# Performance work log

Hardware: AMD Instinct MI355X
Metric: run time of the kernel (lower is better)

## Reference

```python
import jax, jax.numpy as jnp
from jax import lax
import numpy as np

B, T, D, H = 64, 291, 300, 10
K = D // H  # 30
SLOPE = 0.01  # nn.LeakyReLU default
EPS = 1e-5


def _leaky(x):
    return jnp.where(x >= 0, x, SLOPE * x)


def _ln2d(x, g, b):
    # torch LayerNorm over the LAST TWO dims (normalized_shape=[t, d])
    mu = jnp.mean(x, axis=(-2, -1), keepdims=True)
    var = jnp.mean((x - mu) ** 2, axis=(-2, -1), keepdims=True)
    return (x - mu) / jnp.sqrt(var + EPS) * g + b


def _mha(x, Wq, Wk, Wv, Wm):
    # manual multi-head self-attention; q,k each scaled by h**-0.25
    b, t, d = x.shape
    s = H ** 0.25
    q = (x @ Wq.T).reshape(b, t, H, K) / s
    k = (x @ Wk.T).reshape(b, t, H, K) / s
    v = (x @ Wv.T).reshape(b, t, H, K)
    att = jax.nn.softmax(jnp.einsum('bihk,bjhk->bhij', q, k), axis=-1)
    o = jnp.einsum('bhij,bjhk->bihk', att, v).reshape(b, t, d)
    return o @ Wm.T


def _conv_head(R, W, b):
    # Conv2d(2,25,(kh,300)) valid -> [B,25,L,1]; leaky; global maxpool over L
    y = lax.conv_general_dilated(R, W, (1, 1), 'VALID',
                                 dimension_numbers=('NCHW', 'OIHW', 'NCHW'))
    y = _leaky(y + b[None, :, None, None])
    return jnp.max(y, axis=(2, 3))  # [B,25]


def setup_inputs() -> dict:
    key = jax.random.key(0)
    ks = jax.random.split(key, 32)
    it = iter(range(32))
    def n(shape, scale=0.05):
        return (jax.random.normal(ks[next(it)], shape, dtype=jnp.float32) * scale)
    inp = {
        'x1': jax.random.normal(ks[next(it)], (B, T, D), dtype=jnp.float32),
        'x2': jax.random.normal(ks[next(it)], (B, 1000), dtype=jnp.float32),
        'W_img': n((300, 1000)), 'b_img': jnp.zeros((300,), jnp.float32),
        'g1': jnp.ones((T, D), jnp.float32), 'be1': jnp.zeros((T, D), jnp.float32),
        'g2': jnp.ones((1, D), jnp.float32), 'be2': jnp.zeros((1, D), jnp.float32),
        'Wq_tp': n((D, D)), 'Wk_tp': n((D, D)), 'Wv_tp': n((D, D)),
        'Wq_pt': n((D, D)), 'Wk_pt': n((D, D)), 'Wv_pt': n((D, D)),
        'Wq1': n((D, D)), 'Wk1': n((D, D)), 'Wv1': n((D, D)), 'Wm1': n((D, D)),
        'Wq2': n((D, D)), 'Wk2': n((D, D)), 'Wv2': n((D, D)), 'Wm2': n((D, D)),
        'Wq3': n((D, D)), 'Wk3': n((D, D)), 'Wv3': n((D, D)), 'Wm3': n((D, D)),
        'Wc1': n((25, 2, 1, D)), 'Wc2': n((25, 2, 2, D)),
        'Wc3': n((25, 2, 3, D)), 'Wc4': n((25, 2, 4, D)),
        'bc1': jnp.zeros((25,), jnp.float32), 'bc2': jnp.zeros((25,), jnp.float32),
        'bc3': jnp.zeros((25,), jnp.float32), 'bc4': jnp.zeros((25,), jnp.float32),
        'Wlin': n((300, 100)), 'blin': jnp.zeros((300,), jnp.float32),
        'Wlast': n((2, 600)), 'blast': jnp.zeros((2,), jnp.float32),
    }
    return inp


def reference(x1, x2, W_img, b_img, g1, be1, g2, be2,
              Wq_tp, Wk_tp, Wv_tp, Wq_pt, Wk_pt, Wv_pt,
              Wq1, Wk1, Wv1, Wm1, Wq2, Wk2, Wv2, Wm2, Wq3, Wk3, Wv3, Wm3,
              Wc1, Wc2, Wc3, Wc4, bc1, bc2, bc3, bc4,
              Wlin, blin, Wlast, blast):
    # image branch: x2 is the frozen VGG19 1000-d encoding
    img = _leaky(x2 @ W_img.T + b_img)[:, None, :]      # [B,1,300]
    lnP = _ln2d(img, g2, be2)                           # [B,1,300]
    lnT = _ln2d(x1, g1, be1)                            # [B,291,300]

    # cross-attn T->P (query from image, kv from text), unscaled
    q = lnP @ Wq_tp.T; k = lnT @ Wk_tp.T; v = lnT @ Wv_tp.T
    a = jax.nn.softmax(jnp.einsum('bqd,btd->bqt', q, k), axis=-1)
    R_T_P = jnp.einsum('bqt,btd->bqd', a, v) + lnP      # [B,1,300]

    # cross-attn P->T (query from text, kv from image; softmax over size-1 dim)
    q = lnT @ Wq_pt.T; k = lnP @ Wk_pt.T; v = lnP @ Wv_pt.T
    a = jax.nn.softmax(jnp.einsum('btd,bqd->btq', q, k), axis=-1)
    R_P_T = jnp.einsum('btq,bqd->btd', a, v) + lnT      # [B,291,300]

    # 3 stacked multi-head self-attn blocks on the text stream
    a1 = _mha(lnT, Wq1, Wk1, Wv1, Wm1)
    a2 = _mha(a1, Wq2, Wk2, Wv2, Wm2)
    a3 = _mha(a2, Wq3, Wk3, Wv3, Wm3)

    R = jnp.stack((R_P_T, a3), axis=1)                  # [B,2,291,300]
    r1 = _conv_head(R, Wc1, bc1)
    r2 = _conv_head(R, Wc2, bc2)
    r3 = _conv_head(R, Wc3, bc3)
    r4 = _conv_head(R, Wc4, bc4)
    total = jnp.concatenate([r1, r2, r3, r4], axis=1)   # [B,100]
    total = _leaky(total @ Wlin.T + blin)               # [B,300]

    Y = jnp.concatenate([R_T_P[:, 0, :], total], axis=1) @ Wlast.T + blast
    return Y                                            # [B,2]
```

## Files before the change

kernel.cpp:

```cpp
#include <hip/hip_runtime.h>
#include <hip/hip_bf16.h>
#include <math.h>

#define Bn 64
#define Tn 291
#define Dn 300
#define Hn 10
#define Mn (Bn*Tn)
#define Mp 18688
#define Kp 320

typedef __bf16 bf16x8 __attribute__((ext_vector_type(8)));
typedef float f32x4 __attribute__((ext_vector_type(4)));

static __device__ __forceinline__ float leaky(float x){ return x >= 0.f ? x : 0.01f*x; }

template<int NT>
static __device__ __forceinline__ float blockSum(float v, float* red){
  __syncthreads();
  int lane = threadIdx.x & 63, wid = threadIdx.x >> 6;
  #pragma unroll
  for (int o = 32; o > 0; o >>= 1) v += __shfl_down(v, o, 64);
  if (lane == 0) red[wid] = v;
  __syncthreads();
  if (threadIdx.x == 0) {
    float s = red[0];
    #pragma unroll
    for (int w = 1; w < NT/64; ++w) s += red[w];
    red[0] = s;
  }
  __syncthreads();
  return red[0];
}

template<int NT>
static __device__ __forceinline__ float blockMax(float v, float* red){
  __syncthreads();
  int lane = threadIdx.x & 63, wid = threadIdx.x >> 6;
  #pragma unroll
  for (int o = 32; o > 0; o >>= 1) v = fmaxf(v, __shfl_down(v, o, 64));
  if (lane == 0) red[wid] = v;
  __syncthreads();
  if (threadIdx.x == 0) {
    float s = red[0];
    #pragma unroll
    for (int w = 1; w < NT/64; ++w) s = fmaxf(s, red[w]);
    red[0] = s;
  }
  __syncthreads();
  return red[0];
}

__global__ __launch_bounds__(256)
void k_img_lnp(const float* __restrict__ x2, const float* __restrict__ Wimg,
               const float* __restrict__ bimg, const float* __restrict__ g2,
               const float* __restrict__ be2, float* __restrict__ lnP)
{
  int b = blockIdx.x, tid = threadIdx.x;
  __shared__ float sx[1000];
  __shared__ float sy[300];
  __shared__ float red[4];
  for (int i = tid; i < 1000; i += 256) sx[i] = x2[b*1000 + i];
  __syncthreads();
  for (int j = tid; j < 300; j += 256) {
    const float* w = Wimg + j*1000;
    float a = 0.f;
    for (int i = 0; i < 1000; ++i) a += sx[i]*w[i];
    sy[j] = leaky(a + bimg[j]);
  }
  __syncthreads();
  float s = 0.f, ss = 0.f;
  for (int j = tid; j < 300; j += 256) { float v = sy[j]; s += v; ss += v*v; }
  float tot  = blockSum<256>(s, red);
  float tot2 = blockSum<256>(ss, red);
  float mu   = tot * (1.f/300.f);
  float var  = tot2 * (1.f/300.f) - mu*mu;
  float rstd = rsqrtf(var + 1e-5f);
  for (int j = tid; j < 300; j += 256)
    lnP[b*300 + j] = (sy[j]-mu)*rstd*g2[j] + be2[j];
}

__global__ __launch_bounds__(1024)
void k_lnT(const float* __restrict__ x1, const float* __restrict__ g1,
           const float* __restrict__ be1, float* __restrict__ outf,
           __hip_bfloat16* __restrict__ outb)
{
  int b = blockIdx.x, tid = threadIdx.x;
  __shared__ float red[16];
  const float4* xb = (const float4*)(x1 + (size_t)b*87300);
  const float4* g4 = (const float4*)g1;
  const float4* b4 = (const float4*)be1;
  float4* o4 = (float4*)(outf + (size_t)b*87300);
  float s = 0.f, ss = 0.f;
  for (int i = tid; i < 21825; i += 1024) {
    float4 v = xb[i];
    s  += v.x+v.y+v.z+v.w;
    ss += v.x*v.x+v.y*v.y+v.z*v.z+v.w*v.w;
  }
  float tot  = blockSum<1024>(s, red);
  float tot2 = blockSum<1024>(ss, red);
  float mu   = tot / 87300.f;
  float var  = tot2 / 87300.f - mu*mu;
  float rstd = rsqrtf(var + 1e-5f);
  for (int i = tid; i < 21825; i += 1024) {
    float4 v = xb[i], g = g4[i], be = b4[i], o;
    o.x = (v.x-mu)*rstd*g.x + be.x;
    o.y = (v.y-mu)*rstd*g.y + be.y;
    o.z = (v.z-mu)*rstd*g.z + be.z;
    o.w = (v.w-mu)*rstd*g.w + be.w;
    o4[i] = o;
  }
  const float* xs = x1 + (size_t)b*87300;
  for (int e = tid; e < Tn*Dn; e += 1024) {
    int t = e/300;
    float x = xs[e];
    outb[(size_t)(b*Tn+t)*Kp + (e - t*300)] = __float2bfloat16((x-mu)*rstd*g1[e] + be1[e]);
  }
  for (int e = tid; e < Tn*20; e += 1024) {
    int t = e/20, d = 300 + e%20;
    outb[(size_t)(b*Tn+t)*Kp + d] = __float2bfloat16(0.f);
  }
}

__global__ __launch_bounds__(320)
void k_tp(const float* __restrict__ lnP, const float* __restrict__ lnT,
          const float* __restrict__ Wq, const float* __restrict__ Wk,
          const float* __restrict__ Wv, const float* __restrict__ Wvpt,
          float* __restrict__ RTP, float* __restrict__ vpt)
{
  int b = blockIdx.x, tid = threadIdx.x;
  __shared__ float sP[300], sQ[300], sM[300], sA[291], sW[300], red[5];
  if (tid < 300) sP[tid] = lnP[b*300 + tid];
  __syncthreads();
  if (tid < 300) {
    const float* w = Wq + tid*300;
    float a = 0.f;
    for (int i = 0; i < 300; ++i) a += sP[i]*w[i];
    sQ[tid] = a;
  }
  __syncthreads();
  if (tid < 300) {
    float a = 0.f;
    for (int j = 0; j < 300; ++j) a += sQ[j]*Wk[j*300 + tid];
    sM[tid] = a;
  }
  __syncthreads();
  float sc = -1e30f;
  if (tid < 291) {
    const float* r = lnT + ((size_t)b*Tn + tid)*300;
    float a = 0.f;
    for (int i = 0; i < 300; ++i) a += r[i]*sM[i];
    sc = a;
  }
  float mx  = blockMax<320>(sc, red);
  float e   = (tid < 291) ? __expf(sc - mx) : 0.f;
  float den = blockSum<320>(e, red);
  if (tid < 291) sA[tid] = e;
  __syncthreads();
  if (tid < 300) {
    float a = 0.f;
    for (int t = 0; t < 291; ++t) a += sA[t]*lnT[((size_t)b*Tn + t)*300 + tid];
    sW[tid] = a / den;
  }
  __syncthreads();
  if (tid < 300) {
    const float* w = Wv + tid*300;
    float a = 0.f;
    for (int i = 0; i < 300; ++i) a += sW[i]*w[i];
    RTP[b*300 + tid] = a + sP[tid];
    const float* w2 = Wvpt + tid*300;
    float a2 = 0.f;
    for (int i = 0; i < 300; ++i) a2 += sP[i]*w2[i];
    vpt[b*300 + tid] = a2;
  }
}

__global__ __launch_bounds__(256)
void k_rptb(const float* __restrict__ lnT, const float* __restrict__ vpt,
            __hip_bfloat16* __restrict__ out)
{
  int idx = blockIdx.x*256 + threadIdx.x;
  if (idx >= Mn*Kp) return;
  int m = idx / Kp, d = idx - m*Kp;
  int b = m / Tn;
  float v = (d < 300) ? lnT[(size_t)m*300 + d] + vpt[b*300 + d] : 0.f;
  out[idx] = __float2bfloat16(v);
}

struct Wptrs { const float* p[12]; };

__global__ __launch_bounds__(256)
void k_wqkv(Wptrs wp, __hip_bfloat16* __restrict__ out)
{
  int idx = blockIdx.x*256 + threadIdx.x;
  if (idx >= 3*1024*Kp) return;
  int l = idx / (1024*Kp);
  int rem = idx - l*(1024*Kp);
  int rowp = rem / Kp, c = rem - rowp*Kp;
  int hh = rowp >> 5, j = rowp & 31;
  float v = 0.f;
  if (j < 30 && c < 300 && hh < 30) {
    int g = hh/10;
    v = wp.p[l*3 + g][((hh - g*10)*30 + j)*300 + c];
  }
  out[idx] = __float2bfloat16(v);
}

__global__ __launch_bounds__(256)
void k_wcvt(Wptrs wp, __hip_bfloat16* __restrict__ out, int nmat)
{
  int idx = blockIdx.x*256 + threadIdx.x;
  if (idx >= nmat*Kp*Kp) return;
  int mat = idx / (Kp*Kp);
  int rem = idx - mat*(Kp*Kp);
  int r = rem / Kp, c = rem - r*Kp;
  float v = (r < 300 && c < 300) ? wp.p[mat][r*300 + c] : 0.f;
  out[idx] = __float2bfloat16(v);
}

__global__ __launch_bounds__(256)
void k_wpackb(const float* __restrict__ Wc1, const float* __restrict__ Wc2,
              const float* __restrict__ Wc3, const float* __restrict__ Wc4,
              __hip_bfloat16* __restrict__ out)
{
  int idx = blockIdx.x*256 + threadIdx.x;
  if (idx >= 2*256*Kp) return;
  int c  = idx % Kp;
  int rc = idx / Kp;
  int ch = rc / 256;
  int r  = rc % 256;
  float v = 0.f;
  if (r < 250 && c < 300) {
    const float* W; int kh, ro;
    if      (r < 25)  { W = Wc1; kh = 1; ro = r;      }
    else if (r < 75)  { W = Wc2; kh = 2; ro = r - 25; }
    else if (r < 150) { W = Wc3; kh = 3; ro = r - 75; }
    else              { W = Wc4; kh = 4; ro = r - 150;}
    int o = ro/kh, dh = ro%kh;
    v = W[((o*2 + ch)*kh + dh)*300 + c];
  }
  out[idx] = __float2bfloat16(v);
}

template<bool PANEL>
__global__ __launch_bounds__(256)
void k_gemm3(const ushort* __restrict__ A0, const ushort* __restrict__ A1,
             const ushort* __restrict__ W0, const ushort* __restrict__ W1,
             ushort* __restrict__ C0, ushort* __restrict__ C1,
             int nn, int cpitch)
{
  const ushort* A = blockIdx.z ? A1 : A0;
  const ushort* W = blockIdx.z ? W1 : W0;
  ushort*       C = blockIdx.z ? C1 : C0;
  int total = gridDim.x;
  int bid = blockIdx.x;
  int q = total >> 3, r = total & 7;
  int xcd = bid & 7, idx = bid >> 3;
  int wgid = (xcd < r ? xcd*(q+1) : r*(q+1) + (xcd-r)*q) + idx;
  int m0 = (wgid / nn) * 128, n0 = (wgid % nn) * 64;

  __shared__ alignas(16) ushort As[2][128*64];
  __shared__ alignas(16) ushort Bs[2][64*64];
  int tid = threadIdx.x;
  int lane = tid & 63, w = tid >> 6, wr = w >> 1, wc = w & 1;
  int lm = lane & 15, lk = lane >> 4;
  f32x4 acc[4][2] = {};
  uint4 ra[4], rw[2];

  auto loadregs = [&](int kt){
    #pragma unroll
    for (int u = 0; u < 4; ++u) {
      int s = tid + u*256; int row = s >> 3, kg = s & 7;
      ra[u] = *(const uint4*)(A + (size_t)(m0+row)*Kp + kt*64 + kg*8);
    }
    #pragma unroll
    for (int u = 0; u < 2; ++u) {
      int s = tid + u*256; int row = s >> 3, kg = s & 7;
      rw[u] = *(const uint4*)(W + (size_t)(n0+row)*Kp + kt*64 + kg*8);
    }
  };
  auto writeLDS = [&](int buf){
    #pragma unroll
    for (int u = 0; u < 4; ++u) {
      int s = tid + u*256; int row = s >> 3, kg = s & 7;
      *(uint4*)&As[buf][row*64 + ((kg ^ (row&7)) << 3)] = ra[u];
    }
    #pragma unroll
    for (int u = 0; u < 2; ++u) {
      int s = tid + u*256; int row = s >> 3, kg = s & 7;
      *(uint4*)&Bs[buf][row*64 + ((kg ^ (row&7)) << 3)] = rw[u];
    }
  };
  auto compute = [&](int buf){
    #pragma unroll
    for (int s = 0; s < 2; ++s) {
      bf16x8 af[4], bfr[2];
      int kg = s*4 + lk;
      #pragma unroll
      for (int mf = 0; mf < 4; ++mf) {
        int rr = wr*64 + mf*16 + lm;
        af[mf] = *(const bf16x8*)&As[buf][rr*64 + ((kg ^ (rr&7)) << 3)];
      }
      #pragma unroll
      for (int nf = 0; nf < 2; ++nf) {
        int rr = wc*32 + nf*16 + lm;
        bfr[nf] = *(const bf16x8*)&Bs[buf][rr*64 + ((kg ^ (rr&7)) << 3)];
      }
      #pragma unroll
      for (int mf = 0; mf < 4; ++mf)
        #pragma unroll
        for (int nf = 0; nf < 2; ++nf)
          acc[mf][nf] = __builtin_amdgcn_mfma_f32_16x16x32_bf16(af[mf], bfr[nf], acc[mf][nf], 0, 0, 0);
    }
  };

  loadregs(0); writeLDS(0);
  __syncthreads();
  #pragma unroll 1
  for (int kt = 0; kt < 5; ++kt) {
    if (kt < 4) loadregs(kt+1);
    compute(kt & 1);
    if (kt < 4) {
      __syncthreads();
      writeLDS((kt+1) & 1);
      __syncthreads();
    }
  }
  __syncthreads();
  ushort* T = &As[0][0];
  #pragma unroll
  for (int mf = 0; mf < 4; ++mf)
    #pragma unroll
    for (int nf = 0; nf < 2; ++nf)
      #pragma unroll
      for (int i = 0; i < 4; ++i) {
        int rr = wr*64 + mf*16 + lk*4 + i;
        int cc = wc*32 + nf*16 + lm;
        __hip_bfloat16 t = __float2bfloat16(acc[mf][nf][i]);
        T[rr*72 + cc] = *(ushort*)&t;
      }
  __syncthreads();
  #pragma unroll
  for (int u = 0; u < 4; ++u) {
    int s = tid + u*256; int row = s >> 3, g = s & 7;
    uint4 v = *(const uint4*)&T[row*72 + g*8];
    if (PANEL)
      *(uint4*)(C + ((size_t)(n0 >> 6)*Mp + m0 + row)*64 + g*8) = v;
    else
      *(uint4*)(C + (size_t)(m0+row)*cpitch + n0 + g*8) = v;
  }
}

__global__ __launch_bounds__(256)
void k_attn6(const ushort* __restrict__ Xp, ushort* __restrict__ O)
{
  int b = blockIdx.x, h = blockIdx.y, tid = threadIdx.x;
  __shared__ alignas(16) ushort Ks[320*40];
  __shared__ alignas(16) ushort Vt[32*328];
  __shared__ alignas(16) ushort Ps[64*168];
  const size_t rb = (size_t)b*Tn;
  const int Pq = h >> 1, off = (h & 1)*32;
  const int hq = h*30;
  for (int i = tid; i < 320*16; i += 256) {
    int r = i >> 4, c2 = i & 15;
    uint v = (r < Tn) ? *(const uint*)(Xp + ((size_t)(5+Pq)*Mp + rb + r)*64 + off + 2*c2) : 0u;
    *(uint*)&Ks[r*40 + 2*c2] = v;
  }
  for (int i = tid; i < 320*16; i += 256) {
    int j = i >> 4, c2 = i & 15;
    uint v = (j < Tn) ? *(const uint*)(Xp + ((size_t)(10+Pq)*Mp + rb + j)*64 + off + 2*c2) : 0u;
    Vt[(2*c2)*328 + j]   = (ushort)(v & 0xffffu);
    Vt[(2*c2+1)*328 + j] = (ushort)(v >> 16);
  }
  __syncthreads();
  int lane = tid & 63, w = tid >> 6;
  int lm = lane & 15, lk = lane >> 4;
  int qloc = w*16 + lm;
  const float scale = 0.31622776601683794f;
  #pragma unroll 1
  for (int qt = 0; qt < 5; ++qt) {
    int qrow = qt*64 + w*16 + lm;
    union { uint u[4]; bf16x8 v; } qq;
    {
      const uint* qp = (const uint*)(Xp + ((size_t)Pq*Mp + rb + qrow)*64 + off + lk*8);
      qq.u[0]=qp[0]; qq.u[1]=qp[1]; qq.u[2]=qp[2]; qq.u[3]=qp[3];
    }
    bf16x8 qf = qq.v;
    float rsum = 0.f;
    f32x4 oacc[2] = {};
    #pragma unroll 1
    for (int jh = 0; jh < 2; ++jh) {
      #pragma unroll
      for (int jtl = 0; jtl < 10; ++jtl) {
        int jt = jh*10 + jtl;
        bf16x8 kf = *(const bf16x8*)&Ks[(jt*16+lm)*40 + lk*8];
        f32x4 s = {};
        s = __builtin_amdgcn_mfma_f32_16x16x32_bf16(kf, qf, s, 0, 0, 0);
        union { ushort u[4]; uint2 v2; } pk;
        #pragma unroll
        for (int i2 = 0; i2 < 4; ++i2) {
          int j = jt*16 + lk*4 + i2;
          float p = (j < Tn) ? __expf(s[i2]*scale) : 0.f;
          rsum += p;
          __hip_bfloat16 t = __float2bfloat16(p);
          pk.u[i2] = *(ushort*)&t;
        }
        *(uint2*)&Ps[qloc*168 + jtl*16 + lk*4] = pk.v2;
      }
      #pragma unroll
      for (int ktl = 0; ktl < 5; ++ktl) {
        bf16x8 pf = *(const bf16x8*)&Ps[qloc*168 + ktl*32 + lk*8];
        int jb = jh*160 + ktl*32 + lk*8;
        #pragma unroll
        for (int nf = 0; nf < 2; ++nf) {
          bf16x8 vf = *(const bf16x8*)&Vt[(nf*16+lm)*328 + jb];
          oacc[nf] = __builtin_amdgcn_mfma_f32_16x16x32_bf16(pf, vf, oacc[nf], 0, 0, 0);
        }
      }
    }
    rsum += __shfl_xor(rsum, 16, 64);
    rsum += __shfl_xor(rsum, 32, 64);
    float inv[4];
    #pragma unroll
    for (int i2 = 0; i2 < 4; ++i2) inv[i2] = 1.f / __shfl(rsum, lk*4 + i2, 64);
    #pragma unroll
    for (int nf = 0; nf < 2; ++nf) {
      int d = nf*16 + lm;
      if (d < 30) {
        #pragma unroll
        for (int i2 = 0; i2 < 4; ++i2) {
          int qrw = qt*64 + w*16 + lk*4 + i2;
          if (qrw < Tn) {
            __hip_bfloat16 t = __float2bfloat16(oacc[nf][i2]*inv[i2]);
            O[(rb + qrw)*Kp + hq + d] = *(ushort*)&t;
          }
        }
      }
    }
  }
}

__global__ __launch_bounds__(256)
void k_convred2(const ushort* __restrict__ G0, const ushort* __restrict__ G1,
                const float* __restrict__ bc1, const float* __restrict__ bc2,
                const float* __restrict__ bc3, const float* __restrict__ bc4,
                float* __restrict__ out100)
{
  int b = blockIdx.x, head = blockIdx.y;
  int kh  = head + 1;
  int off = (head == 0) ? 0 : (head == 1) ? 25 : (head == 2) ? 75 : 150;
  const float* bc = (head == 0) ? bc1 : (head == 1) ? bc2 : (head == 2) ? bc3 : bc4;
  int ncol = 25*kh;
  int ncp  = ncol | 1;
  int L = Tn - kh + 1;
  __shared__ float S[67*101];
  int tid = threadIdx.x, lane = tid & 63;
  float mx[7];
  #pragma unroll
  for (int u = 0; u < 7; ++u) mx[u] = -1e30f;
  for (int l0 = 0; l0 < L; l0 += 64) {
    int nrows = min(64 + kh - 1, Tn - l0);
    __syncthreads();
    for (int i = tid; i < nrows*ncol; i += 256) {
      int r = i / ncol, c = i % ncol;
      size_t g = (size_t)(b*Tn + l0 + r)*256 + off + c;
      __hip_bfloat16 a = *(const __hip_bfloat16*)&G0[g];
      __hip_bfloat16 d = *(const __hip_bfloat16*)&G1[g];
      S[r*ncp + c] = __bfloat162float(a) + __bfloat162float(d);
    }
    __syncthreads();
    int lmax = min(64, L - l0);
    #pragma unroll
    for (int u = 0; u < 7; ++u) {
      int o = (tid >> 6) + u*4;
      int dl = lane;
      if (o < 25 && dl < lmax) {
        float s = bc[o];
        for (int dh = 0; dh < kh; ++dh)
          s += S[(dl+dh)*ncp + o*kh + dh];
        mx[u] = fmaxf(mx[u], leaky(s));
      }
    }
  }
  #pragma unroll
  for (int u = 0; u < 7; ++u) {
    float v = mx[u];
    #pragma unroll
    for (int ofs = 32; ofs > 0; ofs >>= 1) v = fmaxf(v, __shfl_down(v, ofs, 64));
    int o = (tid >> 6) + u*4;
    if (lane == 0 && o < 25)
      out100[b*100 + head*25 + o] = v;
  }
}

__global__ __launch_bounds__(320)
void k_final(const float* __restrict__ RTP, const float* __restrict__ out100,
             const float* __restrict__ Wlin, const float* __restrict__ blin,
             const float* __restrict__ Wlast, const float* __restrict__ blast,
             float* __restrict__ Y)
{
  int b = blockIdx.x, tid = threadIdx.x;
  __shared__ float cat[600];
  __shared__ float s100[100];
  __shared__ float red[5];
  if (tid < 100) s100[tid] = out100[b*100 + tid];
  if (tid < 300) cat[tid] = RTP[b*300 + tid];
  __syncthreads();
  if (tid < 300) {
    const float* w = Wlin + tid*100;
    float a = blin[tid];
    for (int j = 0; j < 100; ++j) a += s100[j]*w[j];
    cat[300 + tid] = leaky(a);
  }
  __syncthreads();
  for (int c = 0; c < 2; ++c) {
    float a = 0.f;
    for (int i = tid; i < 600; i += 320) a += cat[i]*Wlast[c*600 + i];
    a = blockSum<320>(a, red);
    if (tid == 0) Y[b*2 + c] = a + blast[c];
  }
}

extern "C" void kernel_launch(void* const* d_in, const int* in_sizes, int n_in,
                              void* d_out, int out_size, void* d_ws, size_t ws_size,
                              hipStream_t stream)
{
  (void)in_sizes; (void)n_in; (void)out_size; (void)ws_size;
  const float* x1    = (const float*)d_in[0];
  const float* x2    = (const float*)d_in[1];
  const float* Wimg  = (const float*)d_in[2];
  const float* bimg  = (const float*)d_in[3];
  const float* g1    = (const float*)d_in[4];
  const float* be1   = (const float*)d_in[5];
  const float* g2    = (const float*)d_in[6];
  const float* be2   = (const float*)d_in[7];
  const float* Wq_tp = (const float*)d_in[8];
  const float* Wk_tp = (const float*)d_in[9];
  const float* Wv_tp = (const float*)d_in[10];
  const float* Wv_pt = (const float*)d_in[13];
  const float* Wc1 = (const float*)d_in[26];
  const float* Wc2 = (const float*)d_in[27];
  const float* Wc3 = (const float*)d_in[28];
  const float* Wc4 = (const float*)d_in[29];
  const float* bc1 = (const float*)d_in[30];
  const float* bc2 = (const float*)d_in[31];
  const float* bc3 = (const float*)d_in[32];
  const float* bc4 = (const float*)d_in[33];
  const float* Wlin  = (const float*)d_in[34];
  const float* blin  = (const float*)d_in[35];
  const float* Wlast = (const float*)d_in[36];
  const float* blast = (const float*)d_in[37];

  char* base = (char*)d_ws;
  float* lnP    = (float*)(base + 0);
  float* RTP    = (float*)(base + 76800);
  float* vpt    = (float*)(base + 153600);
  float* out100 = (float*)(base + 230400);
  float*  lnTf  = (float*)(base + 262144);
  ushort* X1024 = (ushort*)(base + 262144);
  ushort* G0    = (ushort*)(base + 262144);
  ushort* G1    = (ushort*)(base + 262144 + 9568256);
  ushort* P0    = (ushort*)(base + 38535168);
  ushort* P1    = (ushort*)(base + 50495488);
  ushort* P2    = (ushort*)(base + 62455808);
  ushort* Wpad  = (ushort*)(base + 74416128);
  ushort* Wm    = (ushort*)(base + 76382208);
  ushort* Wpb   = (ushort*)(base + 76996608);
  const int WS = Kp*Kp;

  k_img_lnp<<<Bn, 256, 0, stream>>>(x2, Wimg, bimg, g2, be2, lnP);
  k_lnT<<<Bn, 1024, 0, stream>>>(x1, g1, be1, lnTf, (__hip_bfloat16*)P0);
  k_tp<<<Bn, 320, 0, stream>>>(lnP, lnTf, Wq_tp, Wk_tp, Wv_tp, Wv_pt, RTP, vpt);
  k_rptb<<<(Mn*Kp + 255)/256, 256, 0, stream>>>(lnTf, vpt, (__hip_bfloat16*)P1);

  Wptrs wq;
  wq.p[0]=(const float*)d_in[14]; wq.p[1]=(const float*)d_in[15]; wq.p[2]=(const float*)d_in[16];
  wq.p[3]=(const float*)d_in[18]; wq.p[4]=(const float*)d_in[19]; wq.p[5]=(const float*)d_in[20];
  wq.p[6]=(const float*)d_in[22]; wq.p[7]=(const float*)d_in[23]; wq.p[8]=(const float*)d_in[24];
  k_wqkv<<<(3*1024*Kp + 255)/256, 256, 0, stream>>>(wq, (__hip_bfloat16*)Wpad);
  Wptrs wm;
  wm.p[0]=(const float*)d_in[17]; wm.p[1]=(const float*)d_in[21]; wm.p[2]=(const float*)d_in[25];
  k_wcvt<<<(3*WS + 255)/256, 256, 0, stream>>>(wm, (__hip_bfloat16*)Wm, 3);
  k_wpackb<<<(2*256*Kp + 255)/256, 256, 0, stream>>>(Wc1, Wc2, Wc3, Wc4, (__hip_bfloat16*)Wpb);

  dim3 gqkv(146*16, 1, 1), gproj(146*5, 1, 1), gconv(146*4, 1, 2), gat(Bn, Hn);
  for (int l = 0; l < 3; ++l) {
    const ushort* Wq3 = Wpad + (size_t)l*1024*Kp;
    const ushort* Wm3 = Wm + (size_t)l*WS;
    k_gemm3<true ><<<gqkv, 256, 0, stream>>>(P0, P0, Wq3, Wq3, X1024, X1024, 16, 0);
    k_attn6<<<gat, 256, 0, stream>>>(X1024, P2);
    k_gemm3<false><<<gproj, 256, 0, stream>>>(P2, P2, Wm3, Wm3, P0, P0, 5, 320);
  }
  k_gemm3<false><<<gconv, 256, 0, stream>>>(P1, P0, Wpb, Wpb + 256*Kp, G0, G1, 4, 256);
  k_convred2<<<dim3(Bn,4), 256, 0, stream>>>(G0, G1, bc1, bc2, bc3, bc4, out100);
  k_final<<<Bn, 320, 0, stream>>>(RTP, out100, Wlin, blin, Wlast, blast, (float*)d_out);
}
```

Baseline: 853.0 us.

## Switch activations to 64-column panel layout and rewrite GEMM with resident A tile

All bf16 activation buffers now use a panel-major layout (64-column panels of Mp rows) via a pidx helper, so every producer and consumer is updated. The GEMM is rewritten so each block loads a full 64x320 A tile into LDS once, and each wave loops over 64-wide N panels. B fragments stream directly from global memory into registers with one-step prefetch, and output goes through a small per-wave LDS staging buffer. The aim is to reuse A across all N panels and drop the double-buffered K loop and its barriers. In exchange, B is read from global memory without LDS sharing across waves, and the grid shrinks to a fixed 292x2, which may cut occupancy and parallelism.

```diff
diff --git a/kernel.cpp b/kernel.cpp
--- a/kernel.cpp
+++ b/kernel.cpp
@@ -14,6 +14,10 @@
 typedef float f32x4 __attribute__((ext_vector_type(4)));
 
 static __device__ __forceinline__ float leaky(float x){ return x >= 0.f ? x : 0.01f*x; }
+
+static __device__ __forceinline__ size_t pidx(int m, int c){
+  return ((size_t)(c >> 6)*Mp + m)*64 + (c & 63);
+}
 
 template<int NT>
 static __device__ __forceinline__ float blockSum(float v, float* red){
@@ -112,13 +116,13 @@
   }
   const float* xs = x1 + (size_t)b*87300;
   for (int e = tid; e < Tn*Dn; e += 1024) {
-    int t = e/300;
+    int t = e/300, d = e - t*300;
     float x = xs[e];
-    outb[(size_t)(b*Tn+t)*Kp + (e - t*300)] = __float2bfloat16((x-mu)*rstd*g1[e] + be1[e]);
+    outb[pidx(b*Tn + t, d)] = __float2bfloat16((x-mu)*rstd*g1[e] + be1[e]);
   }
   for (int e = tid; e < Tn*20; e += 1024) {
     int t = e/20, d = 300 + e%20;
-    outb[(size_t)(b*Tn+t)*Kp + d] = __float2bfloat16(0.f);
+    outb[pidx(b*Tn + t, d)] = __float2bfloat16(0.f);
   }
 }
 
@@ -184,7 +188,7 @@
   int m = idx / Kp, d = idx - m*Kp;
   int b = m / Tn;
   float v = (d < 300) ? lnT[(size_t)m*300 + d] + vpt[b*300 + d] : 0.f;
-  out[idx] = __float2bfloat16(v);
+  out[pidx(m, d)] = __float2bfloat16(v);
 }
 
 struct Wptrs { const float* p[12]; };
@@ -242,112 +246,79 @@
   out[idx] = __float2bfloat16(v);
 }
 
-template<bool PANEL>
-__global__ __launch_bounds__(256)
-void k_gemm3(const ushort* __restrict__ A0, const ushort* __restrict__ A1,
+__global__ __launch_bounds__(256)
+void k_gemm4(const ushort* __restrict__ A0, const ushort* __restrict__ A1,
              const ushort* __restrict__ W0, const ushort* __restrict__ W1,
              ushort* __restrict__ C0, ushort* __restrict__ C1,
-             int nn, int cpitch)
+             int pbase_z, int pcnt, int nptot)
 {
   const ushort* A = blockIdx.z ? A1 : A0;
   const ushort* W = blockIdx.z ? W1 : W0;
   ushort*       C = blockIdx.z ? C1 : C0;
-  int total = gridDim.x;
-  int bid = blockIdx.x;
-  int q = total >> 3, r = total & 7;
-  int xcd = bid & 7, idx = bid >> 3;
-  int wgid = (xcd < r ? xcd*(q+1) : r*(q+1) + (xcd-r)*q) + idx;
-  int m0 = (wgid / nn) * 128, n0 = (wgid % nn) * 64;
-
-  __shared__ alignas(16) ushort As[2][128*64];
-  __shared__ alignas(16) ushort Bs[2][64*64];
-  int tid = threadIdx.x;
-  int lane = tid & 63, w = tid >> 6, wr = w >> 1, wc = w & 1;
+  int m0 = blockIdx.x * 64;
+  __shared__ alignas(16) ushort As[64*320];
+  __shared__ alignas(16) ushort Tb[4][16*72];
+  int tid = threadIdx.x, lane = tid & 63, w = tid >> 6;
   int lm = lane & 15, lk = lane >> 4;
-  f32x4 acc[4][2] = {};
-  uint4 ra[4], rw[2];
-
-  auto loadregs = [&](int kt){
-    #pragma unroll
-    for (int u = 0; u < 4; ++u) {
-      int s = tid + u*256; int row = s >> 3, kg = s & 7;
-      ra[u] = *(const uint4*)(A + (size_t)(m0+row)*Kp + kt*64 + kg*8);
-    }
-    #pragma unroll
-    for (int u = 0; u < 2; ++u) {
-      int s = tid + u*256; int row = s >> 3, kg = s & 7;
-      rw[u] = *(const uint4*)(W + (size_t)(n0+row)*Kp + kt*64 + kg*8);
-    }
-  };
-  auto writeLDS = [&](int buf){
-    #pragma unroll
-    for (int u = 0; u < 4; ++u) {
-      int s = tid + u*256; int row = s >> 3, kg = s & 7;
-      *(uint4*)&As[buf][row*64 + ((kg ^ (row&7)) << 3)] = ra[u];
-    }
-    #pragma unroll
-    for (int u = 0; u < 2; ++u) {
-      int s = tid + u*256; int row = s >> 3, kg = s & 7;
-      *(uint4*)&Bs[buf][row*64 + ((kg ^ (row&7)) << 3)] = rw[u];
-    }
-  };
-  auto compute = [&](int buf){
-    #pragma unroll
-    for (int s = 0; s < 2; ++s) {
-      bf16x8 af[4], bfr[2];
-      int kg = s*4 + lk;
+
+  #pragma unroll
+  for (int u = 0; u < 10; ++u) {
+    int s = u*256 + tid;
+    int row = s/40, kg = s%40;
+    uint4 v = *(const uint4*)(A + ((size_t)(kg>>3)*Mp + m0 + row)*64 + (kg&7)*8);
+    int kgs = (kg & ~7) | ((kg ^ row) & 7);
+    *(uint4*)&As[row*320 + kgs*8] = v;
+  }
+  __syncthreads();
+
+  int ps = blockIdx.z * pbase_z;
+  int pe = min(ps + pcnt, nptot);
+  for (int p = ps + w; p < pe; p += 4) {
+    int n0 = p*64;
+    f32x4 acc[4][4] = {};
+    bf16x8 bcur[4], bnxt[4];
+    #pragma unroll
+    for (int nf = 0; nf < 4; ++nf)
+      bcur[nf] = *(const bf16x8*)(W + (size_t)(n0 + nf*16 + lm)*Kp + lk*8);
+    for (int ks = 0; ks < 10; ++ks) {
+      if (ks < 9) {
+        #pragma unroll
+        for (int nf = 0; nf < 4; ++nf)
+          bnxt[nf] = *(const bf16x8*)(W + (size_t)(n0 + nf*16 + lm)*Kp + (ks+1)*32 + lk*8);
+      }
+      bf16x8 af[4];
       #pragma unroll
       for (int mf = 0; mf < 4; ++mf) {
-        int rr = wr*64 + mf*16 + lm;
-        af[mf] = *(const bf16x8*)&As[buf][rr*64 + ((kg ^ (rr&7)) << 3)];
-      }
-      #pragma unroll
-      for (int nf = 0; nf < 2; ++nf) {
-        int rr = wc*32 + nf*16 + lm;
-        bfr[nf] = *(const bf16x8*)&Bs[buf][rr*64 + ((kg ^ (rr&7)) << 3)];
+        int r = mf*16 + lm;
+        int kg = ks*4 + lk;
+        int kgs = (kg & ~7) | ((kg ^ r) & 7);
+        af[mf] = *(const bf16x8*)&As[r*320 + kgs*8];
       }
       #pragma unroll
       for (int mf = 0; mf < 4; ++mf)
         #pragma unroll
-        for (int nf = 0; nf < 2; ++nf)
-          acc[mf][nf] = __builtin_amdgcn_mfma_f32_16x16x32_bf16(af[mf], bfr[nf], acc[mf][nf], 0, 0, 0);
-    }
-  };
-
-  loadregs(0); writeLDS(0);
-  __syncthreads();
-  #pragma unroll 1
-  for (int kt = 0; kt < 5; ++kt) {
-    if (kt < 4) loadregs(kt+1);
-    compute(kt & 1);
-    if (kt < 4) {
-      __syncthreads();
-      writeLDS((kt+1) & 1);
-      __syncthreads();
-    }
-  }
-  __syncthreads();
-  ushort* T = &As[0][0];
-  #pragma unroll
-  for (int mf = 0; mf < 4; ++mf)
-    #pragma unroll
-    for (int nf = 0; nf < 2; ++nf)
-      #pragma unroll
-      for (int i = 0; i < 4; ++i) {
-        int rr = wr*64 + mf*16 + lk*4 + i;
-        int cc = wc*32 + nf*16 + lm;
-        __hip_bfloat16 t = __float2bfloat16(acc[mf][nf][i]);
-        T[rr*72 + cc] = *(ushort*)&t;
-      }
-  __syncthreads();
-  #pragma unroll
-  for (int u = 0; u < 4; ++u) {
-    int s = tid + u*256; int row = s >> 3, g = s & 7;
-    uint4 v = *(const uint4*)&T[row*72 + g*8];
-    if (PANEL)
-      *(uint4*)(C + ((size_t)(n0 >> 6)*Mp + m0 + row)*64 + g*8) = v;
-    else
-      *(uint4*)(C + (size_t)(m0+row)*cpitch + n0 + g*8) = v;
+        for (int nf = 0; nf < 4; ++nf)
+          acc[mf][nf] = __builtin_amdgcn_mfma_f32_16x16x32_bf16(af[mf], bcur[nf], acc[mf][nf], 0, 0, 0);
+      #pragma unroll
+      for (int nf = 0; nf < 4; ++nf) bcur[nf] = bnxt[nf];
+    }
+    #pragma unroll
+    for (int mf = 0; mf < 4; ++mf) {
+      #pragma unroll
+      for (int nf = 0; nf < 4; ++nf)
+        #pragma unroll
+        for (int i = 0; i < 4; ++i) {
+          __hip_bfloat16 t = __float2bfloat16(acc[mf][nf][i]);
+          Tb[w][(lk*4 + i)*72 + nf*16 + lm] = *(ushort*)&t;
+        }
+      #pragma unroll
+      for (int u = 0; u < 2; ++u) {
+        int s2 = u*64 + lane;
+        int row = s2 >> 3, g = s2 & 7;
+        uint4 v = *(const uint4*)&Tb[w][row*72 + g*8];
+        *(uint4*)(C + ((size_t)p*Mp + m0 + mf*16 + row)*64 + g*8) = v;
+      }
+    }
   }
 }
 
@@ -432,7 +403,7 @@
           int qrw = qt*64 + w*16 + lk*4 + i2;
           if (qrw < Tn) {
             __hip_bfloat16 t = __float2bfloat16(oacc[nf][i2]*inv[i2]);
-            O[(rb + qrw)*Kp + hq + d] = *(ushort*)&t;
+            O[pidx(rb + qrw, hq + d)] = *(ushort*)&t;
           }
         }
       }
@@ -463,7 +434,8 @@
     __syncthreads();
     for (int i = tid; i < nrows*ncol; i += 256) {
       int r = i / ncol, c = i % ncol;
-      size_t g = (size_t)(b*Tn + l0 + r)*256 + off + c;
+      int col = off + c;
+      size_t g = pidx(b*Tn + l0 + r, col);
       __hip_bfloat16 a = *(const __hip_bfloat16*)&G0[g];
       __hip_bfloat16 d = *(const __hip_bfloat16*)&G1[g];
       S[r*ncp + c] = __bfloat162float(a) + __bfloat162float(d);
@@ -583,15 +555,15 @@
   k_wcvt<<<(3*WS + 255)/256, 256, 0, stream>>>(wm, (__hip_bfloat16*)Wm, 3);
   k_wpackb<<<(2*256*Kp + 255)/256, 256, 0, stream>>>(Wc1, Wc2, Wc3, Wc4, (__hip_bfloat16*)Wpb);
 
-  dim3 gqkv(146*16, 1, 1), gproj(146*5, 1, 1), gconv(146*4, 1, 2), gat(Bn, Hn);
+  dim3 g2z(292, 1, 2), gat(Bn, Hn);
   for (int l = 0; l < 3; ++l) {
     const ushort* Wq3 = Wpad + (size_t)l*1024*Kp;
     const ushort* Wm3 = Wm + (size_t)l*WS;
-    k_gemm3<true ><<<gqkv, 256, 0, stream>>>(P0, P0, Wq3, Wq3, X1024, X1024, 16, 0);
+    k_gemm4<<<g2z, 256, 0, stream>>>(P0, P0, Wq3, Wq3, X1024, X1024, 8, 8, 16);
     k_attn6<<<gat, 256, 0, stream>>>(X1024, P2);
-    k_gemm3<false><<<gproj, 256, 0, stream>>>(P2, P2, Wm3, Wm3, P0, P0, 5, 320);
-  }
-  k_gemm3<false><<<gconv, 256, 0, stream>>>(P1, P0, Wpb, Wpb + 256*Kp, G0, G1, 4, 256);
+    k_gemm4<<<g2z, 256, 0, stream>>>(P2, P2, Wm3, Wm3, P0, P0, 3, 3, 5);
+  }
+  k_gemm4<<<g2z, 256, 0, stream>>>(P1, P0, Wpb, Wpb + 256*Kp, G0, G1, 0, 4, 4);
   k_convred2<<<dim3(Bn,4), 256, 0, stream>>>(G0, G1, bc1, bc2, bc3, bc4, out100);
   k_final<<<Bn, 320, 0, stream>>>(RTP, out100, Wlin, blin, Wlast, blast, (float*)d_out);
 }
```

Measured after the change: 692.4 us. -18.8%, faster.
